# Kernel optimization log

Measured on AMD Instinct MI355X. Metric: run time of the kernel, lower is better.

The kernel has to match this reference:

```python
import jax, jax.numpy as jnp
import numpy as np

V, H, L, NH, I, P, B, S = 30000, 768, 12, 12, 3072, 512, 8, 512
D = H // NH  # 64, size_per_head
STD = 0.02
LN_EPS = 1e-3  # Keras LayerNormalization default epsilon


def setup_inputs() -> dict:
    key = jax.random.key(0)
    ks = jax.random.split(key, 16)
    n = lambda k, shape: (jax.random.normal(k, shape, jnp.float32) * STD)
    return {
        "input_ids": jax.random.randint(ks[0], (B, S), 0, V, dtype=jnp.int32),
        "input_mask": jnp.ones((B, S), jnp.int32),
        "token_type_ids": jnp.zeros((B, S), jnp.int32),
        "tok_emb": n(ks[1], (V, H)),
        "pos_emb": n(ks[2], (P, H)),
        "type_emb": n(ks[3], (2, H)),
        "emb_ln_g": jnp.ones((H,), jnp.float32),
        "emb_ln_b": jnp.zeros((H,), jnp.float32),
        "Wq": n(ks[4], (L, H, H)), "bq": jnp.zeros((L, H), jnp.float32),
        "Wk": n(ks[5], (L, H, H)), "bk": jnp.zeros((L, H), jnp.float32),
        "Wv": n(ks[6], (L, H, H)), "bv": jnp.zeros((L, H), jnp.float32),
        "Wo": n(ks[7], (L, H, H)), "bo": jnp.zeros((L, H), jnp.float32),
        "ln1_g": jnp.ones((L, H), jnp.float32), "ln1_b": jnp.zeros((L, H), jnp.float32),
        "Wi": n(ks[8], (L, H, I)), "bi": jnp.zeros((L, I), jnp.float32),
        "Wd": n(ks[9], (L, I, H)), "bd": jnp.zeros((L, H), jnp.float32),
        "ln2_g": jnp.ones((L, H), jnp.float32), "ln2_b": jnp.zeros((L, H), jnp.float32),
    }


def layer_norm(x, g, b):
    mu = jnp.mean(x, axis=-1, keepdims=True)
    var = jnp.mean(jnp.square(x - mu), axis=-1, keepdims=True)
    return (x - mu) * jax.lax.rsqrt(var + LN_EPS) * g + b


def bert_forward(input_ids, input_mask, token_type_ids,
                 tok_emb, pos_emb, type_emb, emb_ln_g, emb_ln_b,
                 Wq, bq, Wk, bk, Wv, bv, Wo, bo, ln1_g, ln1_b,
                 Wi, bi, Wd, bd, ln2_g, ln2_b):
    b, s = input_ids.shape
    # embeddings: token + segment + position, then layernorm (dropout off at inference)
    x = tok_emb[input_ids] + type_emb[token_type_ids] + pos_emb[:s][None, :, :]
    x = layer_norm(x, emb_ln_g, emb_ln_b)

    # additive attention bias from 2D mask: (1 - m) * -10000, broadcast over heads/queries
    mask_bias = (1.0 - input_mask.astype(jnp.float32))[:, None, None, :] * -10000.0  # [b,1,1,s]
    scale = 1.0 / np.sqrt(float(D))

    def block(h, p):
        wq, bq_, wk, bk_, wv, bv_, wo, bo_, g1, b1, wi, bi_, wd, bd_, g2, b2 = p
        # QKV projections, split heads -> [b, nh, s, d]
        split = lambda t: t.reshape(b, s, NH, D).transpose(0, 2, 1, 3)
        q = split(h @ wq + bq_)
        k = split(h @ wk + bk_)
        v = split(h @ wv + bv_)
        scores = jnp.einsum('bhqd,bhkd->bhqk', q, k) * scale + mask_bias
        probs = jax.nn.softmax(scores, axis=-1)
        o = jnp.einsum('bhqk,bhkd->bhqd', probs, v)
        o = o.transpose(0, 2, 1, 3).reshape(b, s, H)
        attn = layer_norm(o @ wo + bo_ + h, g1, b1)
        ffn = jax.nn.gelu(attn @ wi + bi_, approximate=False) @ wd + bd_
        out = layer_norm(ffn + attn, g2, b2)
        return out, None

    params = (Wq, bq, Wk, bk, Wv, bv, Wo, bo, ln1_g, ln1_b, Wi, bi, Wd, bd, ln2_g, ln2_b)
    x, _ = jax.lax.scan(block, x, params)
    return x


def reference(input_ids, input_mask, token_type_ids,
              tok_emb, pos_emb, type_emb, emb_ln_g, emb_ln_b,
              Wq, bq, Wk, bk, Wv, bv, Wo, bo, ln1_g, ln1_b,
              Wi, bi, Wd, bd, ln2_g, ln2_b):
    return bert_forward(input_ids, input_mask, token_type_ids,
                        tok_emb, pos_emb, type_emb, emb_ln_g, emb_ln_b,
                        Wq, bq, Wk, bk, Wv, bv, Wo, bo, ln1_g, ln1_b,
                        Wi, bi, Wd, bd, ln2_g, ln2_b)
```

## Files before the change

kernel.cpp:

```cpp
#include <hip/hip_runtime.h>
#include <math.h>

#define NHEADS 12
#define DHEAD  64
#define SEQL   512
#define HID    768
#define IMID   3072
#define NTOK   4096
#define NLAY   12

typedef __attribute__((ext_vector_type(8))) short short8;
typedef __attribute__((ext_vector_type(4))) float f32x4;

__device__ __forceinline__ short f2b(float f) {
    union { float f; unsigned u; } v; v.f = f;
    unsigned r = (v.u + 0x7fffu + ((v.u >> 16) & 1u)) >> 16;
    return (short)r;
}
__device__ __forceinline__ float b2f(short h) {
    union { unsigned u; float f; } v; v.u = ((unsigned)(unsigned short)h) << 16;
    return v.f;
}
__device__ __forceinline__ void mfma16(f32x4& c, short8 a, short8 b) {
    asm volatile("v_mfma_f32_16x16x32_bf16 %0, %1, %2, %0" : "+v"(c) : "v"(a), "v"(b));
}
__device__ __forceinline__ void accfence() {
    __builtin_amdgcn_sched_barrier(0);
    asm volatile("s_nop 7\ns_nop 7\ns_nop 7\ns_nop 7");
    __builtin_amdgcn_sched_barrier(0);
}
__device__ __forceinline__ void gload_lds16(const void* g, void* l) {
    __builtin_amdgcn_global_load_lds(
        (const __attribute__((address_space(1))) unsigned int*)g,
        (__attribute__((address_space(3))) unsigned int*)l, 16, 0, 0);
}

__global__ __launch_bounds__(256) void wconv_k(
    const float* __restrict__ src, short* __restrict__ dst,
    int K, int N, size_t dlsz, int rowStart)
{
    __shared__ short t[64][72];
    src += (size_t)blockIdx.z * K * N;
    dst += (size_t)blockIdx.z * dlsz;
    const int k0 = blockIdx.x * 64, n0 = blockIdx.y * 64;
    const int kr = threadIdx.x >> 2, q = threadIdx.x & 3;
    const float* s = src + (size_t)(k0 + kr) * N + n0 + q * 16;
#pragma unroll
    for (int j = 0; j < 16; j += 4) {
        float4 v = *reinterpret_cast<const float4*>(s + j);
        t[q * 16 + j + 0][kr] = f2b(v.x);
        t[q * 16 + j + 1][kr] = f2b(v.y);
        t[q * 16 + j + 2][kr] = f2b(v.z);
        t[q * 16 + j + 3][kr] = f2b(v.w);
    }
    __syncthreads();
    const int r = threadIdx.x >> 2;
    short* d = dst + (size_t)(rowStart + n0 + r) * K + k0 + q * 16;
    *reinterpret_cast<short8*>(d)     = *reinterpret_cast<short8*>(&t[r][q * 16]);
    *reinterpret_cast<short8*>(d + 8) = *reinterpret_cast<short8*>(&t[r][q * 16 + 8]);
}

__global__ __launch_bounds__(256) void bpack_k(
    const float* __restrict__ bq, const float* __restrict__ bk,
    const float* __restrict__ bv, float* __restrict__ dst)
{
    int i = blockIdx.x * 256 + threadIdx.x;
    if (i >= NLAY * 2304) return;
    int l = i / 2304, c = i % 2304;
    float v = c < 768 ? bq[l * 768 + c] : c < 1536 ? bk[l * 768 + c - 768] : bv[l * 768 + c - 1536];
    dst[i] = v;
}

__global__ __launch_bounds__(256) void embed_ln_k(
    const int* __restrict__ ids, const int* __restrict__ tti,
    const float* __restrict__ tokE, const float* __restrict__ posE,
    const float* __restrict__ typE, const float* __restrict__ g,
    const float* __restrict__ bb, float* __restrict__ x, short* __restrict__ xb)
{
    __shared__ float red[8];
    const int t = blockIdx.x, s = t & (SEQL - 1);
    const int id = ids[t], ty = tti[t];
    float v[3], sum = 0.f, sq = 0.f;
#pragma unroll
    for (int i = 0; i < 3; ++i) {
        const int c = threadIdx.x + 256 * i;
        float e = tokE[(size_t)id * HID + c] + typE[(size_t)ty * HID + c]
                + posE[(size_t)s * HID + c];
        v[i] = e; sum += e; sq += e * e;
    }
#pragma unroll
    for (int d = 1; d < 64; d <<= 1) { sum += __shfl_xor(sum, d); sq += __shfl_xor(sq, d); }
    const int lane = threadIdx.x & 63, w = threadIdx.x >> 6;
    if (lane == 0) { red[w] = sum; red[4 + w] = sq; }
    __syncthreads();
    sum = red[0] + red[1] + red[2] + red[3];
    sq  = red[4] + red[5] + red[6] + red[7];
    const float mu = sum * (1.0f / 768.0f);
    const float var = sq * (1.0f / 768.0f) - mu * mu;
    const float rstd = rsqrtf(var + 1e-3f);
#pragma unroll
    for (int i = 0; i < 3; ++i) {
        const int c = threadIdx.x + 256 * i;
        float yv = (v[i] - mu) * rstd * g[c] + bb[c];
        x[(size_t)t * HID + c] = yv;
        xb[(size_t)t * HID + c] = f2b(yv);
    }
}

__global__ __launch_bounds__(256) void add_ln_k(
    const float* __restrict__ y, const float* __restrict__ res,
    const float* __restrict__ g, const float* __restrict__ bb,
    float* __restrict__ xout, short* __restrict__ bout, float* __restrict__ fout)
{
    __shared__ float red[8];
    const int t = blockIdx.x;
    float v[3], sum = 0.f, sq = 0.f;
#pragma unroll
    for (int i = 0; i < 3; ++i) {
        const int c = threadIdx.x + 256 * i;
        float e = y[(size_t)t * HID + c] + res[(size_t)t * HID + c];
        v[i] = e; sum += e; sq += e * e;
    }
#pragma unroll
    for (int d = 1; d < 64; d <<= 1) { sum += __shfl_xor(sum, d); sq += __shfl_xor(sq, d); }
    const int lane = threadIdx.x & 63, w = threadIdx.x >> 6;
    if (lane == 0) { red[w] = sum; red[4 + w] = sq; }
    __syncthreads();
    sum = red[0] + red[1] + red[2] + red[3];
    sq  = red[4] + red[5] + red[6] + red[7];
    const float mu = sum * (1.0f / 768.0f);
    const float var = sq * (1.0f / 768.0f) - mu * mu;
    const float rstd = rsqrtf(var + 1e-3f);
#pragma unroll
    for (int i = 0; i < 3; ++i) {
        const int c = threadIdx.x + 256 * i;
        float yv = (v[i] - mu) * rstd * g[c] + bb[c];
        xout[(size_t)t * HID + c] = yv;
        bout[(size_t)t * HID + c] = f2b(yv);
        if (fout) fout[(size_t)t * HID + c] = yv;
    }
}

__global__ __launch_bounds__(256) void add_ln_red_k(
    const float* __restrict__ p0, const float* __restrict__ p1,
    const float* __restrict__ res, const float* __restrict__ g,
    const float* __restrict__ bb, float* __restrict__ xout,
    short* __restrict__ bout, float* __restrict__ fout)
{
    __shared__ float red[8];
    const int t = blockIdx.x;
    float v[3], sum = 0.f, sq = 0.f;
#pragma unroll
    for (int i = 0; i < 3; ++i) {
        const int c = threadIdx.x + 256 * i;
        const size_t o = (size_t)t * HID + c;
        float e = p0[o] + p1[o] + res[o];
        v[i] = e; sum += e; sq += e * e;
    }
#pragma unroll
    for (int d = 1; d < 64; d <<= 1) { sum += __shfl_xor(sum, d); sq += __shfl_xor(sq, d); }
    const int lane = threadIdx.x & 63, w = threadIdx.x >> 6;
    if (lane == 0) { red[w] = sum; red[4 + w] = sq; }
    __syncthreads();
    sum = red[0] + red[1] + red[2] + red[3];
    sq  = red[4] + red[5] + red[6] + red[7];
    const float mu = sum * (1.0f / 768.0f);
    const float var = sq * (1.0f / 768.0f) - mu * mu;
    const float rstd = rsqrtf(var + 1e-3f);
#pragma unroll
    for (int i = 0; i < 3; ++i) {
        const int c = threadIdx.x + 256 * i;
        float yv = (v[i] - mu) * rstd * g[c] + bb[c];
        xout[(size_t)t * HID + c] = yv;
        bout[(size_t)t * HID + c] = f2b(yv);
        if (fout) fout[(size_t)t * HID + c] = yv;
    }
}

template<int EPI>
__global__ __launch_bounds__(256) void gemm3_k(
    const short* __restrict__ A, const short* __restrict__ Wt,
    const float* __restrict__ bias, void* __restrict__ Out, int K, int N, int kChunk,
    void* __restrict__ Out2)
{
    __shared__ short sA[2][128 * 32];
    __shared__ short sB[2][128 * 32];
    const int tid = threadIdx.x;
    const int lane = tid & 63, wave = tid >> 6;
    const int wm = wave >> 1, wn = wave & 1;
    const int rl = lane & 15, hi = lane >> 4;

    const int nb = gridDim.x, bid = blockIdx.x;
    const int id = (bid & 7) * (nb >> 3) + (bid >> 3);
    const int m0 = (id & 31) * 128, n0 = (id >> 5) * 128;
    const int kBeg = blockIdx.y * kChunk;

    f32x4 acc[4][4];
#pragma unroll
    for (int i = 0; i < 4; ++i)
#pragma unroll
        for (int j = 0; j < 4; ++j)
            acc[i][j] = (f32x4){0.f, 0.f, 0.f, 0.f};

    auto stage = [&](int buf, int k0) {
#pragma unroll
        for (int i = 0; i < 2; ++i) {
            const int gb = wave * 128 + i * 64;
            const int gid = gb + lane;
            const int row = gid >> 2, sg = gid & 3;
            const int ksw = (sg ^ ((row >> 1) & 3)) << 3;
            gload_lds16(&A[(size_t)(m0 + row) * K + k0 + ksw], &sA[buf][gb * 8]);
            gload_lds16(&Wt[(size_t)(n0 + row) * K + k0 + ksw], &sB[buf][gb * 8]);
        }
    };

    const int nIter = kChunk >> 5;
    stage(0, kBeg);
    for (int t = 0; t < nIter; ++t) {
        const int cur = t & 1;
        if (t + 1 < nIter) {
            stage(cur ^ 1, kBeg + (t + 1) * 32);
            __builtin_amdgcn_sched_barrier(0);
            asm volatile("s_waitcnt vmcnt(4)" ::: "memory");
        } else {
            __builtin_amdgcn_sched_barrier(0);
            asm volatile("s_waitcnt vmcnt(0)" ::: "memory");
        }
        __builtin_amdgcn_s_barrier();
        __builtin_amdgcn_sched_barrier(0);

        short8 af[4], bfr[4];
#pragma unroll
        for (int f = 0; f < 4; ++f) {
            const int ra = wm * 64 + f * 16 + rl;
            const int rb = wn * 64 + f * 16 + rl;
            af[f]  = *reinterpret_cast<const short8*>(&sA[cur][ra * 32 + ((hi ^ ((ra >> 1) & 3)) << 3)]);
            bfr[f] = *reinterpret_cast<const short8*>(&sB[cur][rb * 32 + ((hi ^ ((rb >> 1) & 3)) << 3)]);
        }
#pragma unroll
        for (int i = 0; i < 4; ++i)
#pragma unroll
            for (int j = 0; j < 4; ++j)
                mfma16(acc[i][j], af[i], bfr[j]);

        asm volatile("s_waitcnt lgkmcnt(0)" ::: "memory");
        __builtin_amdgcn_sched_barrier(0);
        __builtin_amdgcn_s_barrier();
    }
    accfence();
#pragma unroll
    for (int j = 0; j < 4; ++j) {
        const int col = n0 + wn * 64 + j * 16 + rl;
        const float bv = (EPI == 6 && blockIdx.y != 0) ? 0.f : bias[col];
#pragma unroll
        for (int i = 0; i < 4; ++i) {
#pragma unroll
            for (int e = 0; e < 4; ++e) {
                const int row = m0 + wm * 64 + i * 16 + hi * 4 + e;
                float v = acc[i][j][e] + bv;
                if (EPI == 0) {
                    ((float*)Out)[(size_t)row * N + col] = v;
                } else if (EPI == 1) {
                    float gl = 0.5f * v * (1.0f + erff(v * 0.70710678118f));
                    ((short*)Out)[(size_t)row * N + col] = f2b(gl);
                } else if (EPI == 6) {
                    float* dst = blockIdx.y ? (float*)Out2 : (float*)Out;
                    dst[(size_t)row * N + col] = v;
                } else {
                    const int sec = col >= 1536 ? 2 : (col >= 768 ? 1 : 0);
                    const int cc = col - sec * 768;
                    const int b = row >> 9, s = row & 511, nh = cc >> 6, d = cc & 63;
                    short* o = (short*)Out + (size_t)sec * 3145728;
                    if (sec == 2)
                        o[(((size_t)(b * NHEADS + nh) * DHEAD + d) << 9) + s] = f2b(v);
                    else
                        o[(((size_t)(b * NHEADS + nh) * SEQL + s) << 6) + d] = f2b(sec == 0 ? v * 0.125f : v);
                }
            }
        }
    }
}

template<int EPI>
__global__ __launch_bounds__(256) void gemm_k(
    const short* __restrict__ A, const float* __restrict__ W,
    const float* __restrict__ bias, void* __restrict__ Out, int K, int N)
{
    __shared__ short sA[128 * 40];
    __shared__ short sB[128 * 40];
    const int tid = threadIdx.x;
    const int lane = tid & 63, wave = tid >> 6;
    const int wm = wave >> 1, wn = wave & 1;
    const int m0 = blockIdx.x * 128, n0 = blockIdx.y * 128;
    const int rl = lane & 15, hi = lane >> 4;

    f32x4 acc[4][4];
#pragma unroll
    for (int i = 0; i < 4; ++i)
#pragma unroll
        for (int j = 0; j < 4; ++j)
            acc[i][j] = (f32x4){0.f, 0.f, 0.f, 0.f};

    const int arow = tid >> 2, ac8 = (tid & 3) << 3;
    const int bk0 = tid >> 5, bn4 = (tid & 31) << 2;

    for (int k0 = 0; k0 < K; k0 += 32) {
#pragma unroll
        for (int i = 0; i < 2; ++i) {
            int row = i * 64 + arow;
            short8 v = *reinterpret_cast<const short8*>(&A[(size_t)(m0 + row) * K + k0 + ac8]);
            *reinterpret_cast<short8*>(&sA[row * 40 + ac8]) = v;
        }
#pragma unroll
        for (int p = 0; p < 4; ++p) {
            int kk = p * 8 + bk0;
            float4 w4 = *reinterpret_cast<const float4*>(&W[(size_t)(k0 + kk) * N + n0 + bn4]);
            sB[(bn4 + 0) * 40 + kk] = f2b(w4.x);
            sB[(bn4 + 1) * 40 + kk] = f2b(w4.y);
            sB[(bn4 + 2) * 40 + kk] = f2b(w4.z);
            sB[(bn4 + 3) * 40 + kk] = f2b(w4.w);
        }
        __syncthreads();
        short8 af[4], bfr[4];
#pragma unroll
        for (int f = 0; f < 4; ++f) {
            af[f]  = *reinterpret_cast<const short8*>(&sA[(wm * 64 + f * 16 + rl) * 40 + hi * 8]);
            bfr[f] = *reinterpret_cast<const short8*>(&sB[(wn * 64 + f * 16 + rl) * 40 + hi * 8]);
        }
#pragma unroll
        for (int i = 0; i < 4; ++i)
#pragma unroll
            for (int j = 0; j < 4; ++j)
                mfma16(acc[i][j], af[i], bfr[j]);
        __syncthreads();
    }
    accfence();
#pragma unroll
    for (int j = 0; j < 4; ++j) {
        const int col = n0 + wn * 64 + j * 16 + rl;
        const float bv = bias[col];
#pragma unroll
        for (int i = 0; i < 4; ++i) {
#pragma unroll
            for (int e = 0; e < 4; ++e) {
                const int row = m0 + wm * 64 + i * 16 + hi * 4 + e;
                float v = acc[i][j][e] + bv;
                if (EPI == 0) {
                    ((float*)Out)[(size_t)row * N + col] = v;
                } else if (EPI == 1) {
                    float gl = 0.5f * v * (1.0f + erff(v * 0.70710678118f));
                    ((short*)Out)[(size_t)row * N + col] = f2b(gl);
                } else {
                    const int b = row >> 9, s = row & 511, nh = col >> 6, d = col & 63;
                    if (EPI == 2)
                        ((short*)Out)[(((size_t)(b * NHEADS + nh) * SEQL + s) << 6) + d] = f2b(v * 0.125f);
                    else if (EPI == 3)
                        ((short*)Out)[(((size_t)(b * NHEADS + nh) * SEQL + s) << 6) + d] = f2b(v);
                    else
                        ((short*)Out)[(((size_t)(b * NHEADS + nh) * DHEAD + d) << 9) + s] = f2b(v);
                }
            }
        }
    }
}

__global__ __launch_bounds__(256) void attn_k(
    const short* __restrict__ q, const short* __restrict__ k,
    const short* __restrict__ vt, const int* __restrict__ mask,
    short* __restrict__ ctx)
{
    __shared__ short sQ[32 * 72];
    __shared__ short sP[32 * 520];
    __shared__ float wredm[128];
    __shared__ float wreds[128];

    const int blk = blockIdx.x;
    const int qb = blk & 15, bh = blk >> 4;
    const int b = bh / NHEADS, h = bh % NHEADS;
    const int tid = threadIdx.x, lane = tid & 63, wave = tid >> 6;
    const int rl = lane & 15, hi = lane >> 4;
    const short* __restrict__ qh = q + (size_t)bh * SEQL * DHEAD;
    const short* __restrict__ kh = k + (size_t)bh * SEQL * DHEAD;
    const short* __restrict__ vh = vt + (size_t)bh * DHEAD * SEQL;

    {
        int row = tid >> 3, c8 = (tid & 7) << 3;
        *reinterpret_cast<short8*>(&sQ[row * 72 + c8]) =
            *reinterpret_cast<const short8*>(&qh[(size_t)(qb * 32 + row) * DHEAD + c8]);
    }
    __syncthreads();

    f32x4 sacc[2][8];
#pragma unroll
    for (int mf = 0; mf < 2; ++mf)
#pragma unroll
        for (int fn = 0; fn < 8; ++fn)
            sacc[mf][fn] = (f32x4){0.f, 0.f, 0.f, 0.f};
#pragma unroll
    for (int ks = 0; ks < 2; ++ks) {
        short8 a0 = *reinterpret_cast<const short8*>(&sQ[rl * 72 + ks * 32 + hi * 8]);
        short8 a1 = *reinterpret_cast<const short8*>(&sQ[(16 + rl) * 72 + ks * 32 + hi * 8]);
#pragma unroll
        for (int fn = 0; fn < 8; ++fn) {
            int n = wave * 128 + fn * 16 + rl;
            short8 bk = *reinterpret_cast<const short8*>(&kh[(size_t)n * DHEAD + ks * 32 + hi * 8]);
            mfma16(sacc[0][fn], a0, bk);
            mfma16(sacc[1][fn], a1, bk);
        }
    }
    accfence();

    float mb[8];
#pragma unroll
    for (int fn = 0; fn < 8; ++fn) {
        int n = wave * 128 + fn * 16 + rl;
        mb[fn] = -10000.0f * (1.0f - (float)mask[b * SEQL + n]);
    }
#pragma unroll
    for (int mf = 0; mf < 2; ++mf)
#pragma unroll
        for (int fn = 0; fn < 8; ++fn)
#pragma unroll
            for (int e = 0; e < 4; ++e)
                sacc[mf][fn][e] += mb[fn];

    float rmax[2][4];
#pragma unroll
    for (int mf = 0; mf < 2; ++mf)
#pragma unroll
        for (int e = 0; e < 4; ++e) {
            float m = sacc[mf][0][e];
#pragma unroll
            for (int fn = 1; fn < 8; ++fn) m = fmaxf(m, sacc[mf][fn][e]);
            rmax[mf][e] = m;
        }
#pragma unroll
    for (int d = 1; d < 16; d <<= 1)
#pragma unroll
        for (int mf = 0; mf < 2; ++mf)
#pragma unroll
            for (int e = 0; e < 4; ++e)
                rmax[mf][e] = fmaxf(rmax[mf][e], __shfl_xor(rmax[mf][e], d));
    if (rl == 0) {
#pragma unroll
        for (int mf = 0; mf < 2; ++mf)
#pragma unroll
            for (int e = 0; e < 4; ++e)
                wredm[wave * 32 + mf * 16 + hi * 4 + e] = rmax[mf][e];
    }
    __syncthreads();
    float mx[2][4];
#pragma unroll
    for (int mf = 0; mf < 2; ++mf)
#pragma unroll
        for (int e = 0; e < 4; ++e) {
            const int row = mf * 16 + hi * 4 + e;
            float m = wredm[row];
            m = fmaxf(m, wredm[32 + row]);
            m = fmaxf(m, wredm[64 + row]);
            m = fmaxf(m, wredm[96 + row]);
            mx[mf][e] = m;
        }

    float rsum[2][4] = {{0.f, 0.f, 0.f, 0.f}, {0.f, 0.f, 0.f, 0.f}};
#pragma unroll
    for (int mf = 0; mf < 2; ++mf)
#pragma unroll
        for (int fn = 0; fn < 8; ++fn)
#pragma unroll
            for (int e = 0; e < 4; ++e) {
                float p = expf(sacc[mf][fn][e] - mx[mf][e]);
                short hb = f2b(p);
                rsum[mf][e] += b2f(hb);
                sP[(mf * 16 + hi * 4 + e) * 520 + wave * 128 + fn * 16 + rl] = hb;
            }
#pragma unroll
    for (int d = 1; d < 16; d <<= 1)
#pragma unroll
        for (int mf = 0; mf < 2; ++mf)
#pragma unroll
            for (int e = 0; e < 4; ++e)
                rsum[mf][e] += __shfl_xor(rsum[mf][e], d);
    if (rl == 0) {
#pragma unroll
        for (int mf = 0; mf < 2; ++mf)
#pragma unroll
            for (int e = 0; e < 4; ++e)
                wreds[wave * 32 + mf * 16 + hi * 4 + e] = rsum[mf][e];
    }
    __syncthreads();
    float rsf[2][4];
#pragma unroll
    for (int mf = 0; mf < 2; ++mf)
#pragma unroll
        for (int e = 0; e < 4; ++e) {
            const int row = mf * 16 + hi * 4 + e;
            rsf[mf][e] = wreds[row] + wreds[32 + row] + wreds[64 + row] + wreds[96 + row];
        }

    f32x4 oacc[2];
    oacc[0] = (f32x4){0.f, 0.f, 0.f, 0.f};
    oacc[1] = (f32x4){0.f, 0.f, 0.f, 0.f};
#pragma unroll
    for (int ks = 0; ks < 16; ++ks) {
        short8 p0 = *reinterpret_cast<const short8*>(&sP[rl * 520 + ks * 32 + hi * 8]);
        short8 p1 = *reinterpret_cast<const short8*>(&sP[(16 + rl) * 520 + ks * 32 + hi * 8]);
        short8 bv = *reinterpret_cast<const short8*>(&vh[(size_t)(wave * 16 + rl) * SEQL + ks * 32 + hi * 8]);
        mfma16(oacc[0], p0, bv);
        mfma16(oacc[1], p1, bv);
    }
    accfence();
#pragma unroll
    for (int mf = 0; mf < 2; ++mf)
#pragma unroll
        for (int e = 0; e < 4; ++e) {
            const int row = mf * 16 + hi * 4 + e;
            const int s = qb * 32 + row;
            const int d = wave * 16 + rl;
            float o = oacc[mf][e] / rsf[mf][e];
            ctx[((size_t)(b * SEQL + s)) * HID + h * DHEAD + d] = f2b(o);
        }
}

extern "C" void kernel_launch(void* const* d_in, const int* in_sizes, int n_in,
                              void* d_out, int out_size, void* d_ws, size_t ws_size,
                              hipStream_t stream)
{
    const int*   ids  = (const int*)d_in[0];
    const int*   msk  = (const int*)d_in[1];
    const int*   tti  = (const int*)d_in[2];
    const float* tokE = (const float*)d_in[3];
    const float* posE = (const float*)d_in[4];
    const float* typE = (const float*)d_in[5];
    const float* elg  = (const float*)d_in[6];
    const float* elb  = (const float*)d_in[7];
    const float* Wq   = (const float*)d_in[8];  const float* bq = (const float*)d_in[9];
    const float* Wk   = (const float*)d_in[10]; const float* bk = (const float*)d_in[11];
    const float* Wv   = (const float*)d_in[12]; const float* bv = (const float*)d_in[13];
    const float* Wo   = (const float*)d_in[14]; const float* bo = (const float*)d_in[15];
    const float* g1   = (const float*)d_in[16]; const float* b1 = (const float*)d_in[17];
    const float* Wi   = (const float*)d_in[18]; const float* bi = (const float*)d_in[19];
    const float* Wd   = (const float*)d_in[20]; const float* bd = (const float*)d_in[21];
    const float* g2   = (const float*)d_in[22]; const float* b2 = (const float*)d_in[23];

    if (ws_size < 81788928u) return;
    char* ws = (char*)d_ws;
    float* x   = (float*)(ws);
    float* y   = (float*)(ws + 12582912);
    short* xb  = (short*)(ws + 25165824);
    short* qq  = (short*)(ws + 31457280);
    short* kk_ = (short*)(ws + 37748736);
    short* vv  = (short*)(ws + 44040192);
    short* ctx = (short*)(ws + 50331648);
    short* f1  = (short*)(ws + 56623104);
    float* pp  = (float*)(ws + 31457280);

    embed_ln_k<<<NTOK, 256, 0, stream>>>(ids, tti, tokE, posE, typE, elg, elb, x, xb);

    const bool fast = ws_size >= 251768832u;
    if (fast) {
        short* qkvT = (short*)(ws + 81788928);
        short* woT  = (short*)(ws + 124256256);
        short* wiT  = (short*)(ws + 138412032);
        short* wdT  = (short*)(ws + 195035136);
        float* bqkv = (float*)(ws + 251658240);

        wconv_k<<<dim3(12, 12, NLAY), 256, 0, stream>>>(Wq, qkvT, 768, 768, 2304 * 768, 0);
        wconv_k<<<dim3(12, 12, NLAY), 256, 0, stream>>>(Wk, qkvT, 768, 768, 2304 * 768, 768);
        wconv_k<<<dim3(12, 12, NLAY), 256, 0, stream>>>(Wv, qkvT, 768, 768, 2304 * 768, 1536);
        wconv_k<<<dim3(12, 12, NLAY), 256, 0, stream>>>(Wo, woT, 768, 768, 768 * 768, 0);
        wconv_k<<<dim3(12, 48, NLAY), 256, 0, stream>>>(Wi, wiT, 768, 3072, 3072 * 768, 0);
        wconv_k<<<dim3(48, 12, NLAY), 256, 0, stream>>>(Wd, wdT, 3072, 768, 768 * 3072, 0);
        bpack_k<<<108, 256, 0, stream>>>(bq, bk, bv, bqkv);

        for (int l = 0; l < NLAY; ++l) {
            const size_t oH = (size_t)l * HID, oI = (size_t)l * IMID;
            gemm3_k<5><<<dim3(576, 1), 256, 0, stream>>>(xb, qkvT + (size_t)l * 2304 * 768,
                                                         bqkv + (size_t)l * 2304, qq, 768, 2304, 768, nullptr);
            attn_k<<<1536, 256, 0, stream>>>(qq, kk_, vv, msk, ctx);
            gemm3_k<6><<<dim3(192, 2), 256, 0, stream>>>(ctx, woT + (size_t)l * 768 * 768,
                                                         bo + oH, y, 768, 768, 384, pp);
            add_ln_red_k<<<NTOK, 256, 0, stream>>>(y, pp, x, g1 + oH, b1 + oH, x, xb, nullptr);
            gemm3_k<1><<<dim3(768, 1), 256, 0, stream>>>(xb, wiT + (size_t)l * 3072 * 768,
                                                         bi + oI, f1, 768, 3072, 768, nullptr);
            gemm3_k<6><<<dim3(192, 2), 256, 0, stream>>>(f1, wdT + (size_t)l * 768 * 3072,
                                                         bd + oH, y, 3072, 768, 1536, pp);
            add_ln_red_k<<<NTOK, 256, 0, stream>>>(y, pp, x, g2 + oH, b2 + oH, x, xb,
                                                   (l == NLAY - 1) ? (float*)d_out : nullptr);
        }
    } else {
        const dim3 g6(32, 6), g24(32, 24);
        for (int l = 0; l < NLAY; ++l) {
            const size_t oHH = (size_t)l * HID * HID, oH = (size_t)l * HID;
            const size_t oHI = (size_t)l * HID * IMID, oI = (size_t)l * IMID;
            gemm_k<2><<<g6, 256, 0, stream>>>(xb, Wq + oHH, bq + oH, qq, HID, HID);
            gemm_k<3><<<g6, 256, 0, stream>>>(xb, Wk + oHH, bk + oH, kk_, HID, HID);
            gemm_k<4><<<g6, 256, 0, stream>>>(xb, Wv + oHH, bv + oH, vv, HID, HID);
            attn_k<<<1536, 256, 0, stream>>>(qq, kk_, vv, msk, ctx);
            gemm_k<0><<<g6, 256, 0, stream>>>(ctx, Wo + oHH, bo + oH, y, HID, HID);
            add_ln_k<<<NTOK, 256, 0, stream>>>(y, x, g1 + oH, b1 + oH, x, xb, nullptr);
            gemm_k<1><<<g24, 256, 0, stream>>>(xb, Wi + oHI, bi + oI, f1, HID, IMID);
            gemm_k<0><<<g6, 256, 0, stream>>>(f1, Wd + oHI, bd + oH, y, IMID, HID);
            add_ln_k<<<NTOK, 256, 0, stream>>>(y, x, g2 + oH, b2 + oH, x, xb,
                                               (l == NLAY - 1) ? (float*)d_out : nullptr);
        }
    }
}
```

Baseline: 2.539 ms.

## Split FFN down-projection K three ways and tune attention softmax/priority

The FFN down-projection GEMM now splits K into three chunks instead of two, using 576 blocks to fill more CUs. A new add_ln_red3 kernel sums the three partial outputs with the residual before the layernorm. Separately, the attention kernel loads the mask bias before the barrier, raises wave priority around the MFMA loops, and swaps expf and the division for fast __expf and a reciprocal. The trade-offs are an extra fp32 partial buffer to write and read back, and slightly less accurate exp and reciprocal.

```diff
diff --git a/kernel.cpp b/kernel.cpp
--- a/kernel.cpp
+++ b/kernel.cpp
@@ -177,11 +177,47 @@
     }
 }
 
+__global__ __launch_bounds__(256) void add_ln_red3_k(
+    const float* __restrict__ p0, const float* __restrict__ p1,
+    const float* __restrict__ p2, const float* __restrict__ res,
+    const float* __restrict__ g, const float* __restrict__ bb,
+    float* __restrict__ xout, short* __restrict__ bout, float* __restrict__ fout)
+{
+    __shared__ float red[8];
+    const int t = blockIdx.x;
+    float v[3], sum = 0.f, sq = 0.f;
+#pragma unroll
+    for (int i = 0; i < 3; ++i) {
+        const int c = threadIdx.x + 256 * i;
+        const size_t o = (size_t)t * HID + c;
+        float e = p0[o] + p1[o] + p2[o] + res[o];
+        v[i] = e; sum += e; sq += e * e;
+    }
+#pragma unroll
+    for (int d = 1; d < 64; d <<= 1) { sum += __shfl_xor(sum, d); sq += __shfl_xor(sq, d); }
+    const int lane = threadIdx.x & 63, w = threadIdx.x >> 6;
+    if (lane == 0) { red[w] = sum; red[4 + w] = sq; }
+    __syncthreads();
+    sum = red[0] + red[1] + red[2] + red[3];
+    sq  = red[4] + red[5] + red[6] + red[7];
+    const float mu = sum * (1.0f / 768.0f);
+    const float var = sq * (1.0f / 768.0f) - mu * mu;
+    const float rstd = rsqrtf(var + 1e-3f);
+#pragma unroll
+    for (int i = 0; i < 3; ++i) {
+        const int c = threadIdx.x + 256 * i;
+        float yv = (v[i] - mu) * rstd * g[c] + bb[c];
+        xout[(size_t)t * HID + c] = yv;
+        bout[(size_t)t * HID + c] = f2b(yv);
+        if (fout) fout[(size_t)t * HID + c] = yv;
+    }
+}
+
 template<int EPI>
 __global__ __launch_bounds__(256) void gemm3_k(
     const short* __restrict__ A, const short* __restrict__ Wt,
     const float* __restrict__ bias, void* __restrict__ Out, int K, int N, int kChunk,
-    void* __restrict__ Out2)
+    void* __restrict__ Out2, void* __restrict__ Out3)
 {
     __shared__ short sA[2][128 * 32];
     __shared__ short sB[2][128 * 32];
@@ -248,6 +284,9 @@
         __builtin_amdgcn_s_barrier();
     }
     accfence();
+    float* skDst = nullptr;
+    if (EPI == 6)
+        skDst = blockIdx.y == 0 ? (float*)Out : (blockIdx.y == 1 ? (float*)Out2 : (float*)Out3);
 #pragma unroll
     for (int j = 0; j < 4; ++j) {
         const int col = n0 + wn * 64 + j * 16 + rl;
@@ -264,8 +303,7 @@
                     float gl = 0.5f * v * (1.0f + erff(v * 0.70710678118f));
                     ((short*)Out)[(size_t)row * N + col] = f2b(gl);
                 } else if (EPI == 6) {
-                    float* dst = blockIdx.y ? (float*)Out2 : (float*)Out;
-                    dst[(size_t)row * N + col] = v;
+                    skDst[(size_t)row * N + col] = v;
                 } else {
                     const int sec = col >= 1536 ? 2 : (col >= 768 ? 1 : 0);
                     const int cc = col - sec * 768;
@@ -388,6 +426,13 @@
         *reinterpret_cast<short8*>(&sQ[row * 72 + c8]) =
             *reinterpret_cast<const short8*>(&qh[(size_t)(qb * 32 + row) * DHEAD + c8]);
     }
+
+    float mb[8];
+#pragma unroll
+    for (int fn = 0; fn < 8; ++fn) {
+        int n = wave * 128 + fn * 16 + rl;
+        mb[fn] = -10000.0f * (1.0f - (float)mask[b * SEQL + n]);
+    }
     __syncthreads();
 
     f32x4 sacc[2][8];
@@ -396,6 +441,7 @@
 #pragma unroll
         for (int fn = 0; fn < 8; ++fn)
             sacc[mf][fn] = (f32x4){0.f, 0.f, 0.f, 0.f};
+    __builtin_amdgcn_s_setprio(1);
 #pragma unroll
     for (int ks = 0; ks < 2; ++ks) {
         short8 a0 = *reinterpret_cast<const short8*>(&sQ[rl * 72 + ks * 32 + hi * 8]);
@@ -408,14 +454,9 @@
             mfma16(sacc[1][fn], a1, bk);
         }
     }
+    __builtin_amdgcn_s_setprio(0);
     accfence();
 
-    float mb[8];
-#pragma unroll
-    for (int fn = 0; fn < 8; ++fn) {
-        int n = wave * 128 + fn * 16 + rl;
-        mb[fn] = -10000.0f * (1.0f - (float)mask[b * SEQL + n]);
-    }
 #pragma unroll
     for (int mf = 0; mf < 2; ++mf)
 #pragma unroll
@@ -469,7 +510,7 @@
         for (int fn = 0; fn < 8; ++fn)
 #pragma unroll
             for (int e = 0; e < 4; ++e) {
-                float p = expf(sacc[mf][fn][e] - mx[mf][e]);
+                float p = __expf(sacc[mf][fn][e] - mx[mf][e]);
                 short hb = f2b(p);
                 rsum[mf][e] += b2f(hb);
                 sP[(mf * 16 + hi * 4 + e) * 520 + wave * 128 + fn * 16 + rl] = hb;
@@ -501,6 +542,7 @@
     f32x4 oacc[2];
     oacc[0] = (f32x4){0.f, 0.f, 0.f, 0.f};
     oacc[1] = (f32x4){0.f, 0.f, 0.f, 0.f};
+    __builtin_amdgcn_s_setprio(1);
 #pragma unroll
     for (int ks = 0; ks < 16; ++ks) {
         short8 p0 = *reinterpret_cast<const short8*>(&sP[rl * 520 + ks * 32 + hi * 8]);
@@ -509,17 +551,19 @@
         mfma16(oacc[0], p0, bv);
         mfma16(oacc[1], p1, bv);
     }
+    __builtin_amdgcn_s_setprio(0);
     accfence();
 #pragma unroll
-    for (int mf = 0; mf < 2; ++mf)
+    for (int mf = 0; mf < 2; ++mf) {
 #pragma unroll
         for (int e = 0; e < 4; ++e) {
             const int row = mf * 16 + hi * 4 + e;
             const int s = qb * 32 + row;
             const int d = wave * 16 + rl;
-            float o = oacc[mf][e] / rsf[mf][e];
+            float o = oacc[mf][e] * __builtin_amdgcn_rcpf(rsf[mf][e]);
             ctx[((size_t)(b * SEQL + s)) * HID + h * DHEAD + d] = f2b(o);
         }
+    }
 }
 
 extern "C" void kernel_launch(void* const* d_in, const int* in_sizes, int n_in,
@@ -554,6 +598,7 @@
     short* ctx = (short*)(ws + 50331648);
     short* f1  = (short*)(ws + 56623104);
     float* pp  = (float*)(ws + 31457280);
+    float* pp2 = (float*)(ws + 44040192);
 
     embed_ln_k<<<NTOK, 256, 0, stream>>>(ids, tti, tokE, posE, typE, elg, elb, x, xb);
 
@@ -576,17 +621,19 @@
         for (int l = 0; l < NLAY; ++l) {
             const size_t oH = (size_t)l * HID, oI = (size_t)l * IMID;
             gemm3_k<5><<<dim3(576, 1), 256, 0, stream>>>(xb, qkvT + (size_t)l * 2304 * 768,
-                                                         bqkv + (size_t)l * 2304, qq, 768, 2304, 768, nullptr);
+                                                         bqkv + (size_t)l * 2304, qq, 768, 2304, 768,
+                                                         nullptr, nullptr);
             attn_k<<<1536, 256, 0, stream>>>(qq, kk_, vv, msk, ctx);
             gemm3_k<6><<<dim3(192, 2), 256, 0, stream>>>(ctx, woT + (size_t)l * 768 * 768,
-                                                         bo + oH, y, 768, 768, 384, pp);
+                                                         bo + oH, y, 768, 768, 384, pp, nullptr);
             add_ln_red_k<<<NTOK, 256, 0, stream>>>(y, pp, x, g1 + oH, b1 + oH, x, xb, nullptr);
             gemm3_k<1><<<dim3(768, 1), 256, 0, stream>>>(xb, wiT + (size_t)l * 3072 * 768,
-                                                         bi + oI, f1, 768, 3072, 768, nullptr);
-            gemm3_k<6><<<dim3(192, 2), 256, 0, stream>>>(f1, wdT + (size_t)l * 768 * 3072,
-                                                         bd + oH, y, 3072, 768, 1536, pp);
-            add_ln_red_k<<<NTOK, 256, 0, stream>>>(y, pp, x, g2 + oH, b2 + oH, x, xb,
-                                                   (l == NLAY - 1) ? (float*)d_out : nullptr);
+                                                         bi + oI, f1, 768, 3072, 768,
+                                                         nullptr, nullptr);
+            gemm3_k<6><<<dim3(192, 3), 256, 0, stream>>>(f1, wdT + (size_t)l * 768 * 3072,
+                                                         bd + oH, y, 3072, 768, 1024, pp, pp2);
+            add_ln_red3_k<<<NTOK, 256, 0, stream>>>(y, pp, pp2, x, g2 + oH, b2 + oH, x, xb,
+                                                    (l == NLAY - 1) ? (float*)d_out : nullptr);
         }
     } else {
         const dim3 g6(32, 6), g24(32, 24);
```

Result: no change. 2.522 ms (-0.6%).
